# Optimization experiments

Measured on AMD Instinct MI355X. Metric: run time of the kernel, lower is better.

Reference implementation:

```python
import math
import jax, jax.numpy as jnp
import numpy as np

NH = 2            # n_hashes
BSZ = 128         # bucket size (q_cluster_size == k_cluster_size)
H, E, M = 8, 64, 128   # num_heads, dim_per_head, nb_features
SOFTMAX_TEMP = 1.0 / math.sqrt(E)


def setup_inputs() -> dict:
    rng = jax.random.key(0)
    ks = jax.random.split(rng, 8)
    B, N = 4, 4096
    D = H * E
    return {
        "query": jax.random.normal(ks[0], (B, N, D), jnp.float32),
        "key": jax.random.normal(ks[1], (B, N, D), jnp.float32),
        "value": jax.random.normal(ks[2], (B, N, D), jnp.float32),
        "proj_W": jax.random.normal(ks[3], (M, E), jnp.float32),          # performer random features
        "lsh_alpha": jax.random.normal(ks[4], (E + 2, NH), jnp.float32),  # E2LSH projections (xbox+ adds 2 dims)
        "lsh_beta": jax.random.uniform(ks[5], (1, NH), jnp.float32),      # uniform(0, r=1)
        "out_W": jax.random.normal(ks[6], (E, D), jnp.float32) / math.sqrt(D),
        "out_b": jnp.zeros((E,), jnp.float32),
    }


def _split_heads(x, B, N):
    # b n (h e) -> (b h) n e
    return x.reshape(B, N, H, E).transpose(0, 2, 1, 3).reshape(B * H, N, E)


def _xboxplus(q, k):
    # asymmetric MIPS->L2 transform (XBOXPLUS)
    qn = jnp.linalg.norm(q, axis=-1, keepdims=True)
    kn = jnp.linalg.norm(k, axis=-1, keepdims=True)
    MQ = jnp.max(qn, axis=-2, keepdims=True)
    MK = jnp.max(kn, axis=-2, keepdims=True)
    ext_q = jnp.sqrt(jnp.maximum(MQ ** 2 + MK ** 2 - qn ** 2, 0.0))
    ext_k = jnp.sqrt(jnp.maximum(MQ ** 2 + MK ** 2 - kn ** 2, 0.0))
    q_t = jnp.concatenate([q, ext_q, jnp.zeros_like(qn)], axis=-1)
    k_t = jnp.concatenate([k, jnp.zeros_like(kn), ext_k], axis=-1)
    return q_t, k_t


def _feature_map(x, W, is_query):
    # performer softmax kernel features with separated log-scale
    xt = x * math.sqrt(SOFTMAX_TEMP)
    proj = jnp.einsum('bte,me->btm', xt, W)
    log_phi = proj - 0.5 * jnp.sum(xt * xt, axis=-1, keepdims=True) - 0.5 * math.log(M)
    if is_query:
        stab = jnp.max(log_phi, axis=-1, keepdims=True)           # per-position
    else:
        stab = jnp.max(log_phi, axis=(-1, -2), keepdims=True)     # per-batch
    stab = jax.lax.stop_gradient(stab)
    return jnp.exp(log_phi - stab), stab


def _sort_to_buckets(x, perm):
    # x: (bh, T, d), perm: (NH, bh, T) -> (NH, bh, nbuckets, BSZ, d)
    g = jnp.take_along_axis(x[None], perm[..., None], axis=2)
    nh, bh, T, d = g.shape
    return g.reshape(nh, bh, T // BSZ, BSZ, d)


def reference(query, key, value, proj_W, lsh_alpha, lsh_beta, out_W, out_b):
    B, N, D = query.shape
    q = _split_heads(query, B, N)
    k = _split_heads(key, B, N)
    v = _split_heads(value, B, N)

    # ---- LSH clustering (torch.no_grad in original) ----
    q_t, k_t = _xboxplus(jax.lax.stop_gradient(q), jax.lax.stop_gradient(k))
    q_hash = (q_t @ lsh_alpha + lsh_beta).transpose(2, 0, 1)   # (NH, bh, N)
    k_hash = (k_t @ lsh_alpha + lsh_beta).transpose(2, 0, 1)
    q_pos = jnp.argsort(q_hash, axis=-1)
    k_pos = jnp.argsort(k_hash, axis=-1)

    # ---- Performer linear-attention branch ----
    q_prime, q_ls = _feature_map(q, proj_W, True)
    k_prime, k_ls = _feature_map(k, proj_W, False)
    prime_log_scale = q_ls + k_ls                               # (bh, N, 1)

    qk1 = jnp.einsum('btm,bm->bt', q_prime, k_prime.sum(axis=1))        # normalization
    kv = jnp.einsum('bsm,bsd->bmd', k_prime, v)
    qkv = jnp.einsum('btm,bmd->btd', q_prime, kv)

    # ---- bucketed exact attention correction ----
    s_q = _sort_to_buckets(q, q_pos)
    s_k = _sort_to_buckets(k, k_pos)
    s_v = _sort_to_buckets(v, k_pos)
    s_qp = _sort_to_buckets(q_prime, q_pos)
    s_kp = _sort_to_buckets(k_prime, k_pos)
    s_pls = _sort_to_buckets(prime_log_scale, q_pos)            # (NH, bh, nb, BSZ, 1)

    inner = jnp.einsum('hbnie,hbnje->hbnij', s_q, s_k) * SOFTMAX_TEMP
    dots_prime = jnp.einsum('hbnim,hbnjm->hbnij', s_qp, s_kp)

    q_rev = jnp.argsort(q_pos, axis=-1)
    if NH > 1:
        k_rev = jnp.argsort(k_pos, axis=-1)
        q_bidx = (q_rev // BSZ).transpose(1, 2, 0)  # (bh, N, NH)
        k_bidx = (k_rev // BSZ).transpose(1, 2, 0)
        s_qb = _sort_to_buckets(q_bidx, q_pos)      # (NH, bh, nb, BSZ, NH)
        s_kb = _sort_to_buckets(k_bidx, k_pos)
        dup = jnp.sum(s_qb[..., :, None, :] == s_kb[..., None, :, :], axis=-1).astype(inner.dtype)
        inner = inner - jnp.log(dup)
        dots_prime = dots_prime / dup

    dots_lse = jnp.maximum(jnp.max(inner, axis=-1, keepdims=True), s_pls)
    dots = jnp.exp(inner - dots_lse) - dots_prime * jnp.exp(s_pls - dots_lse)
    dots_sum = dots.sum(axis=-1, keepdims=True)
    so = jnp.einsum('hbnij,hbnjd->hbnid', dots, s_v)

    def unsort(s_x):
        nh, bh, nb, bsz, d = s_x.shape
        return jnp.take_along_axis(s_x.reshape(nh, bh, nb * bsz, d), q_rev[..., None], axis=2)

    o = unsort(so)
    logits = unsort(dots_lse)          # (NH, bh, N, 1)
    dots_sum_u = unsort(dots_sum)

    norm_ls = jax.nn.logsumexp(logits, axis=0)                  # (bh, N, 1)
    probs = jnp.exp(logits - norm_ls[None])
    out_lsh = jnp.sum(o * probs, axis=0)
    prime_scale = jnp.exp(prime_log_scale - norm_ls)
    out = out_lsh + qkv * prime_scale
    normalization = (dots_sum_u * probs).sum(axis=0) + qk1[..., None] * prime_scale
    out_n = out / jnp.maximum(normalization, 1e-6)

    out_n = out_n.reshape(B, H, N, E).transpose(0, 2, 1, 3).reshape(B, N, H * E)
    return out_n @ out_W.T + out_b
```

## Files before the change

### kernel.cpp

```cpp
#include <hip/hip_runtime.h>
#include <math.h>

#define BH 32
#define NSEQ 4096
#define EDIM 64
#define MDIM 128
#define NHASH 2
#define NBUCK 32
#define BSZC 128
#define BB 4
#define HH 8
#define DD 512
#define NCHUNK 16

static constexpr size_t OFF_SQQ  = 0;
static constexpr size_t SZ_ROWD  = (size_t)BH*NSEQ*8;
static constexpr size_t OFF_SQK  = OFF_SQQ + SZ_ROWD;
static constexpr size_t OFF_QH   = OFF_SQK + SZ_ROWD;
static constexpr size_t SZ_HASH  = (size_t)NHASH*BH*NSEQ*8;
static constexpr size_t OFF_KH   = OFF_QH + SZ_HASH;
static constexpr size_t OFF_MAXQ = OFF_KH + SZ_HASH;
static constexpr size_t OFF_MAXK = OFF_MAXQ + 256;
static constexpr size_t OFF_KLS  = OFF_MAXK + 256;
static constexpr size_t OFF_QPOS = OFF_KLS + 256;
static constexpr size_t SZ_POS   = (size_t)NHASH*BH*NSEQ*4;
static constexpr size_t OFF_KPOS = OFF_QPOS + SZ_POS;
static constexpr size_t OFF_QREV = OFF_KPOS + SZ_POS;
static constexpr size_t OFF_KREV = OFF_QREV + SZ_POS;
static constexpr size_t OFF_QP   = OFF_KREV + SZ_POS;
static constexpr size_t SZ_PRIME = (size_t)BH*NSEQ*MDIM*4;
static constexpr size_t OFF_KP   = OFF_QP + SZ_PRIME;
static constexpr size_t OFF_QLS  = OFF_KP + SZ_PRIME;
static constexpr size_t OFF_KV   = OFF_QLS + (size_t)BH*NSEQ*4;
static constexpr size_t OFF_KSUM = OFF_KV + (size_t)BH*MDIM*EDIM*4;
static constexpr size_t OFF_O    = OFF_KSUM + (size_t)BH*MDIM*4;
static constexpr size_t OFF_LSE  = OFF_O + (size_t)NHASH*BH*NSEQ*EDIM*4;
static constexpr size_t OFF_DSUM = OFF_LSE + (size_t)NHASH*BH*NSEQ*4;
static constexpr size_t OFF_OUTN = OFF_DSUM + (size_t)NHASH*BH*NSEQ*4;
static constexpr size_t OFF_PKV  = OFF_OUTN + (size_t)BB*NSEQ*DD*4;
static constexpr size_t OFF_PKS  = OFF_PKV + (size_t)BH*NCHUNK*MDIM*EDIM*4;
static constexpr size_t OFF_PROJ = OFF_PKV;
static constexpr size_t OFF_KPB  = OFF_OUTN;
static constexpr size_t OFF_VB   = OFF_PKV;

#define SQRT_TEMP 0.3535533905932738f
#define HALF_LOG_M 2.4260151319598085f
#define LN2F 0.6931471805599453f

typedef __bf16 bf16_t;
typedef bf16_t bf16x8 __attribute__((ext_vector_type(8)));
typedef bf16_t bf16x4 __attribute__((ext_vector_type(4)));
typedef float  f32x16_t __attribute__((ext_vector_type(16)));
#define Z16 {0.f,0.f,0.f,0.f,0.f,0.f,0.f,0.f,0.f,0.f,0.f,0.f,0.f,0.f,0.f,0.f}

__device__ __forceinline__ unsigned encF(float f){
  unsigned u = __float_as_uint(f);
  return (u & 0x80000000u) ? ~u : (u | 0x80000000u);
}
__device__ __forceinline__ float decF(unsigned e){
  return __uint_as_float((e & 0x80000000u) ? (e ^ 0x80000000u) : ~e);
}

__global__ void k_init(char* __restrict__ ws){
  int idx = blockIdx.x*256 + threadIdx.x;
  if (idx < BH){
    ((unsigned long long*)(ws+OFF_MAXQ))[idx] = 0ull;
    ((unsigned long long*)(ws+OFF_MAXK))[idx] = 0ull;
    ((unsigned*)(ws+OFF_KLS))[idx] = encF(-INFINITY);
  }
}

__global__ __launch_bounds__(256) void k_sumsq(const float* __restrict__ q, const float* __restrict__ k,
                                               const float* __restrict__ alpha, char* __restrict__ ws){
  int p = blockIdx.x*256 + threadIdx.x;
  int bh = p >> 12, t = p & (NSEQ-1);
  int bo = bh >> 3, hh = bh & 7;
  const float* qr = q + ((size_t)bo*NSEQ + t)*DD + hh*EDIM;
  const float* kr = k + ((size_t)bo*NSEQ + t)*DD + hh*EDIM;
  double sq = 0.0, sk = 0.0, a0 = 0.0, a1 = 0.0, c0 = 0.0, c1 = 0.0;
  for (int e = 0; e < EDIM; e++){
    double a = qr[e], b = kr[e];
    double al0 = alpha[e*2+0], al1 = alpha[e*2+1];
    sq = fma(a, a, sq);  sk = fma(b, b, sk);
    a0 = fma(a, al0, a0); a1 = fma(a, al1, a1);
    c0 = fma(b, al0, c0); c1 = fma(b, al1, c1);
  }
  ((double*)(ws+OFF_SQQ))[p] = sq;
  ((double*)(ws+OFF_SQK))[p] = sk;
  double* proj = (double*)(ws+OFF_PROJ);
  proj[p]                       = a0;
  proj[(size_t)BH*NSEQ   + p]   = a1;
  proj[(size_t)BH*NSEQ*2 + p]   = c0;
  proj[(size_t)BH*NSEQ*3 + p]   = c1;
  int lane = threadIdx.x & 63, wid = threadIdx.x >> 6;
  double mq = sq, mk = sk;
  for (int o = 32; o; o >>= 1){ mq = fmax(mq, __shfl_xor(mq, o)); mk = fmax(mk, __shfl_xor(mk, o)); }
  __shared__ double smq[4], smk[4];
  if (!lane){ smq[wid] = mq; smk[wid] = mk; }
  __syncthreads();
  if (!threadIdx.x){
    double a = fmax(fmax(smq[0], smq[1]), fmax(smq[2], smq[3]));
    double b = fmax(fmax(smk[0], smk[1]), fmax(smk[2], smk[3]));
    atomicMax((unsigned long long*)(ws+OFF_MAXQ) + bh, (unsigned long long)__double_as_longlong(a));
    atomicMax((unsigned long long*)(ws+OFF_MAXK) + bh, (unsigned long long)__double_as_longlong(b));
  }
}

__global__ __launch_bounds__(256) void k_hash(const float* __restrict__ alpha, const float* __restrict__ beta,
                                              char* __restrict__ ws){
  int p = blockIdx.x*256 + threadIdx.x;
  int bh = p >> 12;
  double mqk = ((const double*)(ws+OFF_MAXQ))[bh] + ((const double*)(ws+OFF_MAXK))[bh];
  double sq  = ((const double*)(ws+OFF_SQQ))[p];
  double sk  = ((const double*)(ws+OFF_SQK))[p];
  double extq = sqrt(fmax(mqk - sq, 0.0));
  double extk = sqrt(fmax(mqk - sk, 0.0));
  const double* proj = (const double*)(ws+OFF_PROJ);
  double a0 = proj[p];
  double a1 = proj[(size_t)BH*NSEQ   + p];
  double c0 = proj[(size_t)BH*NSEQ*2 + p];
  double c1 = proj[(size_t)BH*NSEQ*3 + p];
  a0 += extq * (double)alpha[64*2+0]; a1 += extq * (double)alpha[64*2+1];
  c0 += extk * (double)alpha[65*2+0]; c1 += extk * (double)alpha[65*2+1];
  double b0 = beta[0], b1 = beta[1];
  double* qh = (double*)(ws+OFF_QH);
  double* kh = (double*)(ws+OFF_KH);
  qh[p] = a0 + b0; qh[(size_t)BH*NSEQ + p] = a1 + b1;
  kh[p] = c0 + b0; kh[(size_t)BH*NSEQ + p] = c1 + b1;
}

__global__ __launch_bounds__(1024) void k_sort(char* __restrict__ ws){
  int row = blockIdx.x;
  bool isK = row >= NHASH*BH;
  int r = isK ? row - NHASH*BH : row;
  const double* hash = (const double*)(ws + (isK ? OFF_KH : OFF_QH)) + (size_t)r*NSEQ;
  int* pos = (int*)(ws + (isK ? OFF_KPOS : OFF_QPOS)) + (size_t)r*NSEQ;
  int* rev = (int*)(ws + (isK ? OFF_KREV : OFF_QREV)) + (size_t)r*NSEQ;
  __shared__ double ks_[NSEQ];
  __shared__ int    is_[NSEQ];
  int tid = threadIdx.x, lane = tid & 63;

  double key[4]; int idx[4];
  #pragma unroll
  for (int m = 0; m < 4; m++){ int i = m*1024 + tid; key[m] = hash[i]; idx[m] = i; }

  #pragma unroll
  for (int k = 2; k <= 64; k <<= 1){
    #pragma unroll
    for (int j = 32; j > 0; j >>= 1){
      if (j > (k >> 1)) continue;
      #pragma unroll
      for (int m = 0; m < 4; m++){
        int i = m*1024 + tid;
        bool up = ((i & k) == 0);
        double pk = __shfl_xor(key[m], j);
        int    pi = __shfl_xor(idx[m], j);
        bool isLower = ((lane & j) == 0);
        double lo = isLower ? key[m] : pk;
        double hi = isLower ? pk : key[m];
        if ((lo > hi) == up){ key[m] = pk; idx[m] = pi; }
      }
    }
  }
  #pragma unroll
  for (int m = 0; m < 4; m++){ int i = m*1024 + tid; ks_[i] = key[m]; is_[i] = idx[m]; }
  __syncthreads();

  for (int k = 128; k <= NSEQ; k <<= 1){
    for (int j = k >> 1; j >= 64; j >>= 1){
      for (int i = tid; i < NSEQ; i += 1024){
        int ixj = i ^ j;
        if (ixj > i){
          double a = ks_[i], b = ks_[ixj];
          bool up = ((i & k) == 0);
          if ((a > b) == up){
            ks_[i] = b; ks_[ixj] = a;
            int tmp = is_[i]; is_[i] = is_[ixj]; is_[ixj] = tmp;
          }
        }
      }
      __syncthreads();
    }
    #pragma unroll
    for (int m = 0; m < 4; m++){ int i = m*1024 + tid; key[m] = ks_[i]; idx[m] = is_[i]; }
    #pragma unroll
    for (int j = 32; j > 0; j >>= 1){
      #pragma unroll
      for (int m = 0; m < 4; m++){
        int i = m*1024 + tid;
        bool up = ((i & k) == 0);
        double pk = __shfl_xor(key[m], j);
        int    pi = __shfl_xor(idx[m], j);
        bool isLower = ((lane & j) == 0);
        double lo = isLower ? key[m] : pk;
        double hi = isLower ? pk : key[m];
        if ((lo > hi) == up){ key[m] = pk; idx[m] = pi; }
      }
    }
    #pragma unroll
    for (int m = 0; m < 4; m++){ int i = m*1024 + tid; ks_[i] = key[m]; is_[i] = idx[m]; }
    __syncthreads();
  }
  for (int i = tid; i < NSEQ; i += 1024){ int t = is_[i]; pos[i] = t; rev[t] = i; }
}

__global__ __launch_bounds__(256) void k_featq(const float* __restrict__ query, const float* __restrict__ projW,
                                               char* __restrict__ ws){
  __shared__ float WT[EDIM*MDIM];
  __shared__ float s_q[4][EDIM];
  int tid = threadIdx.x, lane = tid & 63, wid = tid >> 6;
  for (int l = tid; l < EDIM*MDIM; l += 256) WT[l] = projW[(l & 127)*EDIM + (l >> 7)];
  __syncthreads();
  float* qp  = (float*)(ws+OFF_QP);
  float* qls = (float*)(ws+OFF_QLS);
  for (int it = 0; it < 16; it++){
    int p = blockIdx.x*64 + wid*16 + it;
    int bh = p >> 12, t = p & (NSEQ-1), bo = bh >> 3, hh = bh & 7;
    float xv = query[((size_t)bo*NSEQ + t)*DD + hh*EDIM + lane] * SQRT_TEMP;
    s_q[wid][lane] = xv;
    float ss = xv*xv;
    for (int o = 32; o; o >>= 1) ss += __shfl_xor(ss, o);
    float a0 = 0.f, a1 = 0.f;
    for (int e = 0; e < EDIM; e++){
      float qe = s_q[wid][e];
      a0 = fmaf(qe, WT[e*128 + lane], a0);
      a1 = fmaf(qe, WT[e*128 + 64 + lane], a1);
    }
    float c = 0.5f*ss + HALF_LOG_M;
    float lp0 = a0 - c, lp1 = a1 - c;
    float mx = fmaxf(lp0, lp1);
    for (int o = 32; o; o >>= 1) mx = fmaxf(mx, __shfl_xor(mx, o));
    size_t base = (size_t)p*MDIM;
    qp[base + lane]      = expf(lp0 - mx);
    qp[base + 64 + lane] = expf(lp1 - mx);
    if (!lane) qls[p] = mx;
  }
}

__global__ __launch_bounds__(256) void k_featk(const float* __restrict__ key, const float* __restrict__ projW,
                                               char* __restrict__ ws){
  __shared__ float WT[EDIM*MDIM];
  __shared__ float s_q[4][EDIM];
  int tid = threadIdx.x, lane = tid & 63, wid = tid >> 6;
  for (int l = tid; l < EDIM*MDIM; l += 256) WT[l] = projW[(l & 127)*EDIM + (l >> 7)];
  __syncthreads();
  float* kp = (float*)(ws+OFF_KP);
  int bh0 = (blockIdx.x*64) >> 12;
  float bmax = -INFINITY;
  for (int it = 0; it < 16; it++){
    int p = blockIdx.x*64 + wid*16 + it;
    int bh = p >> 12, t = p & (NSEQ-1), bo = bh >> 3, hh = bh & 7;
    float xv = key[((size_t)bo*NSEQ + t)*DD + hh*EDIM + lane] * SQRT_TEMP;
    s_q[wid][lane] = xv;
    float ss = xv*xv;
    for (int o = 32; o; o >>= 1) ss += __shfl_xor(ss, o);
    float a0 = 0.f, a1 = 0.f;
    for (int e = 0; e < EDIM; e++){
      float qe = s_q[wid][e];
      a0 = fmaf(qe, WT[e*128 + lane], a0);
      a1 = fmaf(qe, WT[e*128 + 64 + lane], a1);
    }
    float c = 0.5f*ss + HALF_LOG_M;
    float lp0 = a0 - c, lp1 = a1 - c;
    size_t base = (size_t)p*MDIM;
    kp[base + lane]      = lp0;
    kp[base + 64 + lane] = lp1;
    float mx = fmaxf(lp0, lp1);
    for (int o = 32; o; o >>= 1) mx = fmaxf(mx, __shfl_xor(mx, o));
    bmax = fmaxf(bmax, mx);
  }
  __shared__ float wm[4];
  if (!lane) wm[wid] = bmax;
  __syncthreads();
  if (!tid){
    float m = fmaxf(fmaxf(wm[0], wm[1]), fmaxf(wm[2], wm[3]));
    atomicMax((unsigned*)(ws+OFF_KLS) + bh0, encF(m));
  }
}

__global__ void k_expk(char* __restrict__ ws){
  size_t idx = (size_t)blockIdx.x*256 + threadIdx.x;
  float4* kp = (float4*)(ws+OFF_KP);
  bf16_t* kpb = (bf16_t*)(ws+OFF_KPB);
  int b = (int)(idx >> 17);
  float stab = decF(((const unsigned*)(ws+OFF_KLS))[b]);
  float4 v = kp[idx];
  v.x = expf(v.x - stab); v.y = expf(v.y - stab);
  v.z = expf(v.z - stab); v.w = expf(v.w - stab);
  kp[idx] = v;
  *(bf16x4*)(kpb + idx*4) = (bf16x4){(bf16_t)v.x,(bf16_t)v.y,(bf16_t)v.z,(bf16_t)v.w};
}

__global__ __launch_bounds__(256, 4) void k_kv(const float* __restrict__ value, char* __restrict__ ws){
  int b = blockIdx.x >> 4;
  int chunk = blockIdx.x & 15;
  int bo = b >> 3, hh = b & 7;
  const float* kp = (const float*)(ws+OFF_KP) + (size_t)b*NSEQ*MDIM;
  __shared__ float skp[32][MDIM];
  __shared__ float sv [32][EDIM];
  int tid = threadIdx.x;
  int d = tid & 63, mg = tid >> 6;
  int m0 = mg*32;
  float acc[32];
  #pragma unroll
  for (int i = 0; i < 32; i++) acc[i] = 0.f;
  float ksacc = 0.f;
  #pragma unroll 1
  for (int s0 = chunk*256; s0 < chunk*256 + 256; s0 += 32){
    __syncthreads();
    {
      const float4* src = (const float4*)(kp + (size_t)s0*MDIM);
      #pragma unroll
      for (int l = tid; l < 32*MDIM/4; l += 256) ((float4*)skp)[l] = src[l];
    }
    #pragma unroll
    for (int l = tid; l < 32*EDIM/4; l += 256){
      int r = l >> 4, c4 = (l & 15) << 2;
      *(float4*)&sv[r][c4] = *(const float4*)(value + ((size_t)bo*NSEQ + s0 + r)*DD + hh*EDIM + c4);
    }
    __syncthreads();
    #pragma unroll 1
    for (int ss = 0; ss < 32; ss += 2){
      float vv0 = sv[ss+0][d];
      float vv1 = sv[ss+1][d];
      #pragma unroll
      for (int mq = 0; mq < 8; mq++){
        float4 k0 = *(const float4*)&skp[ss+0][m0 + mq*4];
        float4 k1 = *(const float4*)&skp[ss+1][m0 + mq*4];
        acc[mq*4+0] = fmaf(k0.x, vv0, acc[mq*4+0]);
        acc[mq*4+1] = fmaf(k0.y, vv0, acc[mq*4+1]);
        acc[mq*4+2] = fmaf(k0.z, vv0, acc[mq*4+2]);
        acc[mq*4+3] = fmaf(k0.w, vv0, acc[mq*4+3]);
        acc[mq*4+0] = fmaf(k1.x, vv1, acc[mq*4+0]);
        acc[mq*4+1] = fmaf(k1.y, vv1, acc[mq*4+1]);
        acc[mq*4+2] = fmaf(k1.z, vv1, acc[mq*4+2]);
        acc[mq*4+3] = fmaf(k1.w, vv1, acc[mq*4+3]);
      }
    }
    if (tid < 128){
      #pragma unroll
      for (int ss = 0; ss < 32; ss++) ksacc += skp[ss][tid];
    }
  }
  float* pkv = (float*)(ws+OFF_PKV) + ((size_t)(b*NCHUNK + chunk)*MDIM + m0)*EDIM + d;
  #pragma unroll
  for (int mi = 0; mi < 32; mi++) pkv[mi*EDIM] = acc[mi];
  if (tid < 128)
    ((float*)(ws+OFF_PKS))[(b*NCHUNK + chunk)*MDIM + tid] = ksacc;
}

__global__ __launch_bounds__(256) void k_kvred(char* __restrict__ ws){
  int blk = blockIdx.x;
  if (blk < 1024){
    int idx = blk*256 + threadIdx.x;
    int b = idx >> 13, rem = idx & 8191;
    const float* pkv = (const float*)(ws+OFF_PKV);
    float s = 0.f;
    #pragma unroll
    for (int c = 0; c < NCHUNK; c++) s += pkv[(((size_t)b*NCHUNK + c) << 13) + rem];
    ((float*)(ws+OFF_KV))[idx] = s;
  } else {
    int j = (blk - 1024)*256 + threadIdx.x;
    const float* pks = (const float*)(ws+OFF_PKS);
    int b = j >> 7, m = j & 127;
    float s = 0.f;
    #pragma unroll
    for (int c = 0; c < NCHUNK; c++) s += pks[(b*NCHUNK + c)*MDIM + m];
    ((float*)(ws+OFF_KSUM))[j] = s;
  }
}

__global__ __launch_bounds__(256) void k_cvtv(const float* __restrict__ value, char* __restrict__ ws){
  bf16_t* vb = (bf16_t*)(ws+OFF_VB);
  size_t idx = (size_t)blockIdx.x*256 + threadIdx.x;
  int e4 = (int)(idx & 15) << 2;
  int t  = (int)((idx >> 4) & 4095);
  int b  = (int)(idx >> 16);
  int bo = b >> 3, hh = b & 7;
  float4 x = *(const float4*)(value + ((size_t)bo*NSEQ + t)*DD + hh*EDIM + e4);
  *(bf16x4*)(vb + ((size_t)b*NSEQ + t)*EDIM + e4) =
      (bf16x4){(bf16_t)x.x,(bf16_t)x.y,(bf16_t)x.z,(bf16_t)x.w};
}

__global__ __launch_bounds__(256, 2) void k_bucket(const float* __restrict__ query,
                                                   const float* __restrict__ key,
                                                   char* __restrict__ ws){
  __shared__ __align__(16) bf16_t s_kT[128*72];
  __shared__ __align__(16) bf16_t s_kp[128*136];
  __shared__ __align__(16) bf16_t s_v [64*136];
  __shared__ int   s_tq[128], s_tk[128], s_qb[128], s_kb[128];
  __shared__ float s_pls[128];

  int blk = blockIdx.x;
  int h = blk >> 10;
  int b = (blk >> 5) & 31;
  int n = blk & 31;
  int tid = threadIdx.x, lane = tid & 63, wid = tid >> 6;
  int col = lane & 31, half = lane >> 5;
  int bo = b >> 3, hh = b & 7;

  const int* kpos  = (const int*)(ws+OFF_KPOS) + ((size_t)h*BH + b)*NSEQ + n*BSZC;
  const int* qpos  = (const int*)(ws+OFF_QPOS) + ((size_t)h*BH + b)*NSEQ + n*BSZC;
  const int* qrev0 = (const int*)(ws+OFF_QREV) + (size_t)b*NSEQ;
  const int* qrev1 = (const int*)(ws+OFF_QREV) + ((size_t)BH + b)*NSEQ;
  const int* krev0 = (const int*)(ws+OFF_KREV) + (size_t)b*NSEQ;
  const int* krev1 = (const int*)(ws+OFF_KREV) + ((size_t)BH + b)*NSEQ;
  const float* qp_g = (const float*)(ws+OFF_QP) + (size_t)b*NSEQ*MDIM;
  const bf16_t* kpb_g = (const bf16_t*)(ws+OFF_KPB) + (size_t)b*NSEQ*MDIM;
  const bf16_t* vb_g  = (const bf16_t*)(ws+OFF_VB)  + (size_t)b*NSEQ*EDIM;
  const float* qls  = (const float*)(ws+OFF_QLS) + (size_t)b*NSEQ;
  float klsb = decF(((const unsigned*)(ws+OFF_KLS))[b]);

  if (tid < 128){
    int t = qpos[tid];
    s_tq[tid]  = t;
    s_pls[tid] = qls[t] + klsb;
    s_qb[tid]  = (qrev0[t] >> 7) | ((qrev1[t] >> 7) << 16);
  } else {
    int j = tid - 128;
    int t = kpos[j];
    s_tk[j] = t;
    s_kb[j] = (krev0[t] >> 7) | ((krev1[t] >> 7) << 16);
  }
  __syncthreads();

  for (int l = tid; l < 128*16; l += 256){
    int j = l >> 4, e4 = (l & 15) << 2;
    int t = s_tk[j];
    float4 x = *(const float4*)(key + ((size_t)bo*NSEQ + t)*DD + hh*EDIM + e4);
    bf16x4 y = {(bf16_t)x.x, (bf16_t)x.y, (bf16_t)x.z, (bf16_t)x.w};
    *(bf16x4*)&s_kT[j*72 + e4] = y;
  }
  for (int l = tid; l < 128*16; l += 256){
    int j = l >> 4, m8 = (l & 15) << 3;
    int t = s_tk[j];
    *(bf16x8*)&s_kp[j*136 + m8] = *(const bf16x8*)(kpb_g + (size_t)t*MDIM + m8);
  }
  for (int l = tid; l < 128*8; l += 256){
    int j = l >> 3, d8 = (l & 7) << 3;
    int t = s_tk[j];
    bf16x8 vv = *(const bf16x8*)(vb_g + (size_t)t*EDIM + d8);
    #pragma unroll
    for (int i = 0; i < 8; i++) s_v[(d8+i)*136 + j] = vv[i];
  }
  __syncthreads();

  float* o_g   = (float*)(ws+OFF_O)    + ((size_t)h*BH + b)*NSEQ*EDIM;
  float* lse_g = (float*)(ws+OFF_LSE)  + ((size_t)h*BH + b)*NSEQ;
  float* dsm_g = (float*)(ws+OFF_DSUM) + ((size_t)h*BH + b)*NSEQ;

  int mrow = wid*32 + col;
  int tq_m = s_tq[mrow];

  const float* qr = query + ((size_t)bo*NSEQ + tq_m)*DD + hh*EDIM + half*8;
  bf16x8 aq[4];
  #pragma unroll
  for (int kb = 0; kb < 4; kb++){
    float4 x0 = *(const float4*)(qr + kb*16);
    float4 x1 = *(const float4*)(qr + kb*16 + 4);
    bf16x8 a = {(bf16_t)x0.x,(bf16_t)x0.y,(bf16_t)x0.z,(bf16_t)x0.w,
                (bf16_t)x1.x,(bf16_t)x1.y,(bf16_t)x1.z,(bf16_t)x1.w};
    aq[kb] = a;
  }
  f32x16_t ain[4] = {Z16, Z16, Z16, Z16};
  #pragma unroll
  for (int jt = 0; jt < 4; jt++){
    #pragma unroll
    for (int kb = 0; kb < 4; kb++){
      bf16x8 bk = *(const bf16x8*)&s_kT[(jt*32 + col)*72 + kb*16 + half*8];
      ain[jt] = __builtin_amdgcn_mfma_f32_32x32x16_bf16(aq[kb], bk, ain[jt], 0, 0, 0);
    }
  }

  const float* qpr = qp_g + (size_t)tq_m*MDIM + half*8;
  bf16x8 aqp[8];
  #pragma unroll
  for (int kb = 0; kb < 8; kb++){
    float4 x0 = *(const float4*)(qpr + kb*16);
    float4 x1 = *(const float4*)(qpr + kb*16 + 4);
    bf16x8 a = {(bf16_t)x0.x,(bf16_t)x0.y,(bf16_t)x0.z,(bf16_t)x0.w,
                (bf16_t)x1.x,(bf16_t)x1.y,(bf16_t)x1.z,(bf16_t)x1.w};
    aqp[kb] = a;
  }
  f32x16_t apr[4] = {Z16, Z16, Z16, Z16};
  #pragma unroll
  for (int jt = 0; jt < 4; jt++){
    #pragma unroll
    for (int kb = 0; kb < 8; kb++){
      bf16x8 bk = *(const bf16x8*)&s_kp[(jt*32 + col)*136 + kb*16 + half*8];
      apr[jt] = __builtin_amdgcn_mfma_f32_32x32x16_bf16(aqp[kb], bk, apr[jt], 0, 0, 0);
    }
  }
  __syncthreads();

  float pls_r[16]; int qb_r[16];
  #pragma unroll
  for (int i = 0; i < 16; i++){
    int r = wid*32 + (i & 3) + 8*(i >> 2) + 4*half;
    pls_r[i] = s_pls[r];
    qb_r[i]  = s_qb[r];
  }
  float mx[16];
  #pragma unroll
  for (int i = 0; i < 16; i++) mx[i] = -INFINITY;
  #pragma unroll
  for (int jt = 0; jt < 4; jt++){
    int kbp = s_kb[jt*32 + col];
    int kb0 = kbp & 0xffff, kb1 = kbp >> 16;
    #pragma unroll
    for (int i = 0; i < 16; i++){
      int dup2 = ((qb_r[i] & 0xffff) == kb0) & ((qb_r[i] >> 16) == kb1);
      float in = ain[jt][i]*0.125f - (dup2 ? LN2F : 0.0f);
      float dp = dup2 ? apr[jt][i]*0.5f : apr[jt][i];
      ain[jt][i] = in; apr[jt][i] = dp;
      mx[i] = fmaxf(mx[i], in);
    }
  }
  #pragma unroll
  for (int i = 0; i < 16; i++){
    #pragma unroll
    for (int o = 16; o; o >>= 1) mx[i] = fmaxf(mx[i], __shfl_xor(mx[i], o));
  }
  float L[16], eps[16], dsum[16];
  #pragma unroll
  for (int i = 0; i < 16; i++){
    L[i] = fmaxf(mx[i], pls_r[i]);
    eps[i] = expf(pls_r[i] - L[i]);
    dsum[i] = 0.f;
  }
  #pragma unroll
  for (int jt = 0; jt < 4; jt++){
    #pragma unroll
    for (int i = 0; i < 16; i++){
      float d = expf(ain[jt][i] - L[i]) - apr[jt][i]*eps[i];
      dsum[i] += d;
      int r = wid*32 + (i & 3) + 8*(i >> 2) + 4*half;
      s_kp[r*136 + jt*32 + col] = (bf16_t)d;
    }
  }
  #pragma unroll
  for (int i = 0; i < 16; i++){
    #pragma unroll
    for (int o = 16; o; o >>= 1) dsum[i] += __shfl_xor(dsum[i], o);
  }
  __syncthreads();

  f32x16_t ao[2] = {Z16, Z16};
  #pragma unroll
  for (int kb = 0; kb < 8; kb++){
    bf16x8 ad = *(const bf16x8*)&s_kp[mrow*136 + kb*16 + half*8];
    #pragma unroll
    for (int dt = 0; dt < 2; dt++){
      bf16x8 bv = *(const bf16x8*)&s_v[(dt*32 + col)*136 + kb*16 + half*8];
      ao[dt] = __builtin_amdgcn_mfma_f32_32x32x16_bf16(ad, bv, ao[dt], 0, 0, 0);
    }
  }

  #pragma unroll
  for (int i = 0; i < 16; i++){
    int r = wid*32 + (i & 3) + 8*(i >> 2) + 4*half;
    int t = s_tq[r];
    o_g[(size_t)t*EDIM + col]      = ao[0][i];
    o_g[(size_t)t*EDIM + 32 + col] = ao[1][i];
    if (col == 0){ lse_g[t] = L[i]; dsm_g[t] = dsum[i]; }
  }
}

__global__ __launch_bounds__(256) void k_combine(char* __restrict__ ws){
  int b = blockIdx.x >> 6;
  int chunk = blockIdx.x & 63;
  int tid = threadIdx.x, lane = tid & 63, wid = tid >> 6;
  __shared__ float s_kv[MDIM*EDIM];
  __shared__ float s_ks[MDIM];
  __shared__ float s_qp[4][MDIM];
  const float* kv = (const float*)(ws+OFF_KV) + (size_t)b*MDIM*EDIM;
  for (int l = tid; l < MDIM*EDIM; l += 256) s_kv[l] = kv[l];
  if (tid < MDIM) s_ks[tid] = ((const float*)(ws+OFF_KSUM))[b*MDIM + tid];
  __syncthreads();
  const float* qp_g  = (const float*)(ws+OFF_QP) + (size_t)b*NSEQ*MDIM;
  const float* qls   = (const float*)(ws+OFF_QLS) + (size_t)b*NSEQ;
  const float* lse_g = (const float*)(ws+OFF_LSE);
  const float* dsm_g = (const float*)(ws+OFF_DSUM);
  const float* o_g   = (const float*)(ws+OFF_O);
  float* outn = (float*)(ws+OFF_OUTN);
  float klsb = decF(((const unsigned*)(ws+OFF_KLS))[b]);
  int bo = b >> 3, hh = b & 7;
  for (int it = 0; it < 16; it++){
    int t = chunk*64 + wid*16 + it;
    float qp0 = qp_g[(size_t)t*MDIM + lane];
    float qp1 = qp_g[(size_t)t*MDIM + 64 + lane];
    s_qp[wid][lane] = qp0; s_qp[wid][64 + lane] = qp1;
    float qkv = 0.f;
    for (int m = 0; m < 128; m++) qkv = fmaf(s_qp[wid][m], s_kv[m*64 + lane], qkv);
    float qk1 = qp0*s_ks[lane] + qp1*s_ks[64 + lane];
    for (int o = 32; o; o >>= 1) qk1 += __shfl_xor(qk1, o);
    size_t pidx = (size_t)b*NSEQ + t;
    float l0 = lse_g[pidx], l1 = lse_g[(size_t)BH*NSEQ + pidx];
    float mx = fmaxf(l0, l1);
    float nls = mx + logf(expf(l0 - mx) + expf(l1 - mx));
    float p0 = expf(l0 - nls), p1 = expf(l1 - nls);
    float ps = expf(qls[t] + klsb - nls);
    float o0 = o_g[pidx*EDIM + lane];
    float o1 = o_g[((size_t)BH*NSEQ + pidx)*EDIM + lane];
    float ds0 = dsm_g[pidx], ds1 = dsm_g[(size_t)BH*NSEQ + pidx];
    float outv = o0*p0 + o1*p1 + qkv*ps;
    float nrm  = ds0*p0 + ds1*p1 + qk1*ps;
    outn[((size_t)bo*NSEQ + t)*DD + hh*EDIM + lane] = outv / fmaxf(nrm, 1e-6f);
  }
}

__global__ __launch_bounds__(256) void k_final(const float* __restrict__ outW, const float* __restrict__ outB,
                                               const char* __restrict__ ws, float* __restrict__ out){
  __shared__ float WT[DD*65];
  __shared__ float s_x[4][DD];
  int tid = threadIdx.x, lane = tid & 63, wid = tid >> 6;
  for (int l = tid; l < EDIM*DD; l += 256){
    int e = l >> 9, d = l & 511;
    WT[d*65 + e] = outW[l];
  }
  __syncthreads();
  const float* outn = (const float*)(ws+OFF_OUTN);
  for (int it = 0; it < 16; it++){
    int p = blockIdx.x*64 + wid*16 + it;
    const float* x = outn + (size_t)p*DD;
    #pragma unroll
    for (int c = 0; c < 8; c++) s_x[wid][c*64 + lane] = x[c*64 + lane];
    float acc = 0.f;
    for (int d = 0; d < DD; d++) acc = fmaf(s_x[wid][d], WT[d*65 + lane], acc);
    out[(size_t)p*EDIM + lane] = acc + outB[lane];
  }
}

extern "C" void kernel_launch(void* const* d_in, const int* in_sizes, int n_in,
                              void* d_out, int out_size, void* d_ws, size_t ws_size,
                              hipStream_t stream) {
  const float* query = (const float*)d_in[0];
  const float* key   = (const float*)d_in[1];
  const float* value = (const float*)d_in[2];
  const float* projW = (const float*)d_in[3];
  const float* alpha = (const float*)d_in[4];
  const float* beta  = (const float*)d_in[5];
  const float* outW  = (const float*)d_in[6];
  const float* outB  = (const float*)d_in[7];
  char* ws = (char*)d_ws;
  float* out = (float*)d_out;

  k_init <<<1,    256, 0, stream>>>(ws);
  k_sumsq<<<512,  256, 0, stream>>>(query, key, alpha, ws);
  k_hash <<<512,  256, 0, stream>>>(alpha, beta, ws);
  k_sort <<<128, 1024, 0, stream>>>(ws);
  k_featq<<<2048, 256, 0, stream>>>(query, projW, ws);
  k_featk<<<2048, 256, 0, stream>>>(key, projW, ws);
  k_expk <<<16384,256, 0, stream>>>(ws);
  k_kv   <<<512,  256, 0, stream>>>(value, ws);
  k_kvred<<<1040, 256, 0, stream>>>(ws);
  k_cvtv <<<8192, 256, 0, stream>>>(value, ws);
  k_bucket<<<2048,256, 0, stream>>>(query, key, ws);
  k_combine<<<2048,256,0, stream>>>(ws);
  k_final<<<256,  256, 0, stream>>>(outW, outB, ws, out);
}
```

Baseline: 746.6 us.

## Fuse feature kernels, move key exp into kv and conversion kernels

```diff
diff --git a/kernel.cpp b/kernel.cpp
--- a/kernel.cpp
+++ b/kernel.cpp
@@ -78,12 +78,19 @@
   const float* qr = q + ((size_t)bo*NSEQ + t)*DD + hh*EDIM;
   const float* kr = k + ((size_t)bo*NSEQ + t)*DD + hh*EDIM;
   double sq = 0.0, sk = 0.0, a0 = 0.0, a1 = 0.0, c0 = 0.0, c1 = 0.0;
-  for (int e = 0; e < EDIM; e++){
-    double a = qr[e], b = kr[e];
-    double al0 = alpha[e*2+0], al1 = alpha[e*2+1];
-    sq = fma(a, a, sq);  sk = fma(b, b, sk);
-    a0 = fma(a, al0, a0); a1 = fma(a, al1, a1);
-    c0 = fma(b, al0, c0); c1 = fma(b, al1, c1);
+  for (int e4 = 0; e4 < EDIM; e4 += 4){
+    float4 qv4 = *(const float4*)(qr + e4);
+    float4 kv4 = *(const float4*)(kr + e4);
+    float qs[4] = {qv4.x, qv4.y, qv4.z, qv4.w};
+    float ks[4] = {kv4.x, kv4.y, kv4.z, kv4.w};
+    #pragma unroll
+    for (int j = 0; j < 4; j++){
+      double a = qs[j], b = ks[j];
+      double al0 = alpha[(e4+j)*2+0], al1 = alpha[(e4+j)*2+1];
+      sq = fma(a, a, sq);  sk = fma(b, b, sk);
+      a0 = fma(a, al0, a0); a1 = fma(a, al1, a1);
+      c0 = fma(b, al0, c0); c1 = fma(b, al1, c1);
+    }
   }
   ((double*)(ws+OFF_SQQ))[p] = sq;
   ((double*)(ws+OFF_SQK))[p] = sk;
@@ -204,8 +211,8 @@
   for (int i = tid; i < NSEQ; i += 1024){ int t = is_[i]; pos[i] = t; rev[t] = i; }
 }
 
-__global__ __launch_bounds__(256) void k_featq(const float* __restrict__ query, const float* __restrict__ projW,
-                                               char* __restrict__ ws){
+__global__ __launch_bounds__(256) void k_feat(const float* __restrict__ query, const float* __restrict__ key,
+                                              const float* __restrict__ projW, char* __restrict__ ws){
   __shared__ float WT[EDIM*MDIM];
   __shared__ float s_q[4][EDIM];
   int tid = threadIdx.x, lane = tid & 63, wid = tid >> 6;
@@ -213,6 +220,7 @@
   __syncthreads();
   float* qp  = (float*)(ws+OFF_QP);
   float* qls = (float*)(ws+OFF_QLS);
+  float* kp  = (float*)(ws+OFF_KP);
   for (int it = 0; it < 16; it++){
     int p = blockIdx.x*64 + wid*16 + it;
     int bh = p >> 12, t = p & (NSEQ-1), bo = bh >> 3, hh = bh & 7;
@@ -235,16 +243,6 @@
     qp[base + 64 + lane] = expf(lp1 - mx);
     if (!lane) qls[p] = mx;
   }
-}
-
-__global__ __launch_bounds__(256) void k_featk(const float* __restrict__ key, const float* __restrict__ projW,
-                                               char* __restrict__ ws){
-  __shared__ float WT[EDIM*MDIM];
-  __shared__ float s_q[4][EDIM];
-  int tid = threadIdx.x, lane = tid & 63, wid = tid >> 6;
-  for (int l = tid; l < EDIM*MDIM; l += 256) WT[l] = projW[(l & 127)*EDIM + (l >> 7)];
-  __syncthreads();
-  float* kp = (float*)(ws+OFF_KP);
   int bh0 = (blockIdx.x*64) >> 12;
   float bmax = -INFINITY;
   for (int it = 0; it < 16; it++){
@@ -278,24 +276,12 @@
   }
 }
 
-__global__ void k_expk(char* __restrict__ ws){
-  size_t idx = (size_t)blockIdx.x*256 + threadIdx.x;
-  float4* kp = (float4*)(ws+OFF_KP);
-  bf16_t* kpb = (bf16_t*)(ws+OFF_KPB);
-  int b = (int)(idx >> 17);
-  float stab = decF(((const unsigned*)(ws+OFF_KLS))[b]);
-  float4 v = kp[idx];
-  v.x = expf(v.x - stab); v.y = expf(v.y - stab);
-  v.z = expf(v.z - stab); v.w = expf(v.w - stab);
-  kp[idx] = v;
-  *(bf16x4*)(kpb + idx*4) = (bf16x4){(bf16_t)v.x,(bf16_t)v.y,(bf16_t)v.z,(bf16_t)v.w};
-}
-
 __global__ __launch_bounds__(256, 4) void k_kv(const float* __restrict__ value, char* __restrict__ ws){
   int b = blockIdx.x >> 4;
   int chunk = blockIdx.x & 15;
   int bo = b >> 3, hh = b & 7;
   const float* kp = (const float*)(ws+OFF_KP) + (size_t)b*NSEQ*MDIM;
+  float stab = decF(((const unsigned*)(ws+OFF_KLS))[b]);
   __shared__ float skp[32][MDIM];
   __shared__ float sv [32][EDIM];
   int tid = threadIdx.x;
@@ -311,7 +297,12 @@
     {
       const float4* src = (const float4*)(kp + (size_t)s0*MDIM);
       #pragma unroll
-      for (int l = tid; l < 32*MDIM/4; l += 256) ((float4*)skp)[l] = src[l];
+      for (int l = tid; l < 32*MDIM/4; l += 256){
+        float4 x = src[l];
+        x.x = expf(x.x - stab); x.y = expf(x.y - stab);
+        x.z = expf(x.z - stab); x.w = expf(x.w - stab);
+        ((float4*)skp)[l] = x;
+      }
     }
     #pragma unroll
     for (int l = tid; l < 32*EDIM/4; l += 256){
@@ -370,16 +361,29 @@
   }
 }
 
-__global__ __launch_bounds__(256) void k_cvtv(const float* __restrict__ value, char* __restrict__ ws){
-  bf16_t* vb = (bf16_t*)(ws+OFF_VB);
-  size_t idx = (size_t)blockIdx.x*256 + threadIdx.x;
-  int e4 = (int)(idx & 15) << 2;
-  int t  = (int)((idx >> 4) & 4095);
-  int b  = (int)(idx >> 16);
-  int bo = b >> 3, hh = b & 7;
-  float4 x = *(const float4*)(value + ((size_t)bo*NSEQ + t)*DD + hh*EDIM + e4);
-  *(bf16x4*)(vb + ((size_t)b*NSEQ + t)*EDIM + e4) =
-      (bf16x4){(bf16_t)x.x,(bf16_t)x.y,(bf16_t)x.z,(bf16_t)x.w};
+__global__ __launch_bounds__(256) void k_cvt(const float* __restrict__ value, char* __restrict__ ws){
+  int blk = blockIdx.x;
+  if (blk < 16384){
+    size_t idx = (size_t)blk*256 + threadIdx.x;
+    const float4* kp = (const float4*)(ws+OFF_KP);
+    bf16_t* kpb = (bf16_t*)(ws+OFF_KPB);
+    int b = (int)(idx >> 17);
+    float stab = decF(((const unsigned*)(ws+OFF_KLS))[b]);
+    float4 v = kp[idx];
+    v.x = expf(v.x - stab); v.y = expf(v.y - stab);
+    v.z = expf(v.z - stab); v.w = expf(v.w - stab);
+    *(bf16x4*)(kpb + idx*4) = (bf16x4){(bf16_t)v.x,(bf16_t)v.y,(bf16_t)v.z,(bf16_t)v.w};
+  } else {
+    bf16_t* vb = (bf16_t*)(ws+OFF_VB);
+    size_t idx = (size_t)(blk - 16384)*256 + threadIdx.x;
+    int e4 = (int)(idx & 15) << 2;
+    int t  = (int)((idx >> 4) & 4095);
+    int b  = (int)(idx >> 16);
+    int bo = b >> 3, hh = b & 7;
+    float4 x = *(const float4*)(value + ((size_t)bo*NSEQ + t)*DD + hh*EDIM + e4);
+    *(bf16x4*)(vb + ((size_t)b*NSEQ + t)*EDIM + e4) =
+        (bf16x4){(bf16_t)x.x,(bf16_t)x.y,(bf16_t)x.z,(bf16_t)x.w};
+  }
 }
 
 __global__ __launch_bounds__(256, 2) void k_bucket(const float* __restrict__ query,
@@ -424,6 +428,23 @@
   }
   __syncthreads();
 
+  int mrow = wid*32 + col;
+  int tq_m = s_tq[mrow];
+  const float* qr  = query + ((size_t)bo*NSEQ + tq_m)*DD + hh*EDIM + half*8;
+  const float* qpr = qp_g + (size_t)tq_m*MDIM + half*8;
+  float4 aqf[8];
+  #pragma unroll
+  for (int kb = 0; kb < 4; kb++){
+    aqf[2*kb]   = *(const float4*)(qr + kb*16);
+    aqf[2*kb+1] = *(const float4*)(qr + kb*16 + 4);
+  }
+  float4 aqpf[16];
+  #pragma unroll
+  for (int kb = 0; kb < 8; kb++){
+    aqpf[2*kb]   = *(const float4*)(qpr + kb*16);
+    aqpf[2*kb+1] = *(const float4*)(qpr + kb*16 + 4);
+  }
+
   for (int l = tid; l < 128*16; l += 256){
     int j = l >> 4, e4 = (l & 15) << 2;
     int t = s_tk[j];
@@ -449,18 +470,12 @@
   float* lse_g = (float*)(ws+OFF_LSE)  + ((size_t)h*BH + b)*NSEQ;
   float* dsm_g = (float*)(ws+OFF_DSUM) + ((size_t)h*BH + b)*NSEQ;
 
-  int mrow = wid*32 + col;
-  int tq_m = s_tq[mrow];
-
-  const float* qr = query + ((size_t)bo*NSEQ + tq_m)*DD + hh*EDIM + half*8;
   bf16x8 aq[4];
   #pragma unroll
   for (int kb = 0; kb < 4; kb++){
-    float4 x0 = *(const float4*)(qr + kb*16);
-    float4 x1 = *(const float4*)(qr + kb*16 + 4);
-    bf16x8 a = {(bf16_t)x0.x,(bf16_t)x0.y,(bf16_t)x0.z,(bf16_t)x0.w,
-                (bf16_t)x1.x,(bf16_t)x1.y,(bf16_t)x1.z,(bf16_t)x1.w};
-    aq[kb] = a;
+    float4 x0 = aqf[2*kb], x1 = aqf[2*kb+1];
+    aq[kb] = (bf16x8){(bf16_t)x0.x,(bf16_t)x0.y,(bf16_t)x0.z,(bf16_t)x0.w,
+                      (bf16_t)x1.x,(bf16_t)x1.y,(bf16_t)x1.z,(bf16_t)x1.w};
   }
   f32x16_t ain[4] = {Z16, Z16, Z16, Z16};
   #pragma unroll
@@ -472,15 +487,12 @@
     }
   }
 
-  const float* qpr = qp_g + (size_t)tq_m*MDIM + half*8;
   bf16x8 aqp[8];
   #pragma unroll
   for (int kb = 0; kb < 8; kb++){
-    float4 x0 = *(const float4*)(qpr + kb*16);
-    float4 x1 = *(const float4*)(qpr + kb*16 + 4);
-    bf16x8 a = {(bf16_t)x0.x,(bf16_t)x0.y,(bf16_t)x0.z,(bf16_t)x0.w,
-                (bf16_t)x1.x,(bf16_t)x1.y,(bf16_t)x1.z,(bf16_t)x1.w};
-    aqp[kb] = a;
+    float4 x0 = aqpf[2*kb], x1 = aqpf[2*kb+1];
+    aqp[kb] = (bf16x8){(bf16_t)x0.x,(bf16_t)x0.y,(bf16_t)x0.z,(bf16_t)x0.w,
+                       (bf16_t)x1.x,(bf16_t)x1.y,(bf16_t)x1.z,(bf16_t)x1.w};
   }
   f32x16_t apr[4] = {Z16, Z16, Z16, Z16};
   #pragma unroll
@@ -649,12 +661,10 @@
   k_sumsq<<<512,  256, 0, stream>>>(query, key, alpha, ws);
   k_hash <<<512,  256, 0, stream>>>(alpha, beta, ws);
   k_sort <<<128, 1024, 0, stream>>>(ws);
-  k_featq<<<2048, 256, 0, stream>>>(query, projW, ws);
-  k_featk<<<2048, 256, 0, stream>>>(key, projW, ws);
-  k_expk <<<16384,256, 0, stream>>>(ws);
+  k_feat <<<2048, 256, 0, stream>>>(query, key, projW, ws);
   k_kv   <<<512,  256, 0, stream>>>(value, ws);
   k_kvred<<<1040, 256, 0, stream>>>(ws);
-  k_cvtv <<<8192, 256, 0, stream>>>(value, ws);
+  k_cvt  <<<24576,256, 0, stream>>>(value, ws);
   k_bucket<<<2048,256, 0, stream>>>(query, key, ws);
   k_combine<<<2048,256,0, stream>>>(ws);
   k_final<<<256,  256, 0, stream>>>(outW, outB, ws, out);
```

After: 714.4 us. -4.3%, faster.
